# Kernel tuning notes

Hardware: AMD Instinct MI355X
Metric: run time of the kernel (lower is better)

The kernel has to match this reference:

```python
import jax, jax.numpy as jnp
import numpy as np

DIM = 768
HEADS = 12
HEAD_DIM = DIM // HEADS  # 64
THETA = 10000.0
B, S = 2, 2048


def rotate_half(x):
    # pairs-interleaved rotate: (x1, x2) -> (-x2, x1)
    xp = x.reshape(x.shape[:-1] + (-1, 2))
    x1, x2 = xp[..., 0], xp[..., 1]
    return jnp.stack((-x2, x1), axis=-1).reshape(x.shape)


def rope_freqs(seq_len, head_dim, dtype):
    inv = 1.0 / (THETA ** (jnp.arange(0, head_dim, 2, dtype=jnp.float32) / head_dim))
    pos = jnp.arange(seq_len, dtype=jnp.float32)
    f = pos[:, None] * inv[None, :]              # [S, head_dim//2]
    f = jnp.repeat(f, 2, axis=-1)                # [S, head_dim]
    return f.astype(dtype)


def apply_rotary(freqs, t):
    # freqs [S, D] broadcasts against t [B, H, S, D]
    return t * jnp.cos(freqs) + rotate_half(t) * jnp.sin(freqs)


def setup_inputs() -> dict:
    key = jax.random.key(0)
    k1, k2, k3 = jax.random.split(key, 3)
    x = jax.random.normal(k1, (B, S, DIM), dtype=jnp.float32)
    W_qkv = jax.random.normal(k2, (3 * DIM, DIM), dtype=jnp.float32) * 0.02
    W_proj = jax.random.normal(k3, (DIM, DIM), dtype=jnp.float32) * 0.02
    b_proj = jnp.zeros((DIM,), dtype=jnp.float32)
    return {"x": x, "W_qkv": W_qkv, "W_proj": W_proj, "b_proj": b_proj}


def reference(x, W_qkv, W_proj, b_proj):
    Bb, Ss, C = x.shape
    qkv = jnp.einsum('bsc,oc->bso', x, W_qkv)                    # [B,S,3C]
    qkv = qkv.reshape(Bb, Ss, 3, HEADS, HEAD_DIM)
    qkv = jnp.transpose(qkv, (2, 0, 3, 1, 4))                    # [3,B,H,S,D]
    q, k, v = qkv[0], qkv[1], qkv[2]
    freqs = rope_freqs(Ss, HEAD_DIM, x.dtype)
    q = apply_rotary(freqs, q)
    k = apply_rotary(freqs, k)
    scale = HEAD_DIM ** -0.5
    scores = jnp.einsum('bhqd,bhkd->bhqk', q, k) * scale         # [B,H,S,S]
    probs = jax.nn.softmax(scores, axis=-1)
    out = jnp.einsum('bhqk,bhkd->bhqd', probs, v)                # [B,H,S,D]
    out = jnp.transpose(out, (0, 2, 1, 3)).reshape(Bb, Ss, C)
    return jnp.einsum('bsc,oc->bso', out, W_proj) + b_proj
```

## Files before the change

kernel.cpp:

```cpp
#include <hip/hip_runtime.h>
#include <math.h>

#define Bq 2
#define Sq 2048
#define Cq 768
#define Hq 12
#define Dq 64

#define PANEL_SHORTS 98304
#define PANELS_X  32
#define PANELS_WQ 18
#define PANELS_WP 6

#define NROWS 49152
#define OPHALF 3145728

typedef _Float16 f16x8 __attribute__((ext_vector_type(8)));
typedef __fp16 fp16v2 __attribute__((ext_vector_type(2)));
typedef float f32x4 __attribute__((ext_vector_type(4)));
#define MFMA16F(a, b, c) __builtin_amdgcn_mfma_f32_16x16x32_f16(a, b, c, 0, 0, 0)

#define SCALEQ 0.18033688011112042f

static __device__ inline unsigned short f16bits(float x) {
    _Float16 h = (_Float16)x;
    return __builtin_bit_cast(unsigned short, h);
}
static __device__ inline unsigned int pk16(float a, float b) {
    fp16v2 h = __builtin_amdgcn_cvt_pkrtz(a, b);
    return __builtin_bit_cast(unsigned int, h);
}

static __device__ inline void gld_lds16(const unsigned short* g, unsigned short* l) {
    __builtin_amdgcn_global_load_lds(
        (const __attribute__((address_space(1))) unsigned int*)g,
        (__attribute__((address_space(3))) unsigned int*)l, 16, 0, 0);
}

__global__ void freq_kernel(float* __restrict__ ctab, float* __restrict__ stab) {
    int idx = blockIdx.x * blockDim.x + threadIdx.x;
    int s = idx >> 5;
    int i = idx & 31;
    double f = (double)s * exp(-(double)i * 0.28782313662425573);
    ctab[idx] = (float)cos(f);
    stab[idx] = (float)sin(f);
}

__global__ __launch_bounds__(256) void split_kernel(
    const float* __restrict__ x, const float* __restrict__ wq,
    const float* __restrict__ wp,
    unsigned short* __restrict__ xs, unsigned short* __restrict__ wqs,
    unsigned short* __restrict__ wps)
{
    const int cid  = blockIdx.x * 256 + threadIdx.x;
    const int panel = cid / 12288;
    const int pos8  = cid % 12288;
    const int step = pos8 >> 10;
    const int rem  = pos8 & 1023;
    const int J    = rem >> 6;
    const int lane = rem & 63;
    const int rowp = J * 8 + (lane >> 3);
    const int lc   = (lane & 7) ^ (rowp & 7);
    const int k    = step * 64 + lc * 8;
    const float* src; unsigned short* dst; int prow;
    if (panel < PANELS_X) {
        src = x;  dst = xs;  prow = panel;
    } else if (panel < PANELS_X + PANELS_WQ) {
        src = wq; dst = wqs; prow = panel - PANELS_X;
    } else {
        src = wp; dst = wps; prow = panel - PANELS_X - PANELS_WQ;
    }
    const int row = prow * 128 + rowp;
    float4 v0 = *(const float4*)(src + (size_t)row * Cq + k);
    float4 v1 = *(const float4*)(src + (size_t)row * Cq + k + 4);
    unsigned short o[8] = { f16bits(v0.x), f16bits(v0.y), f16bits(v0.z),
                            f16bits(v0.w), f16bits(v1.x), f16bits(v1.y),
                            f16bits(v1.z), f16bits(v1.w) };
    *(uint4*)&dst[(size_t)prow * PANEL_SHORTS + (size_t)pos8 * 8] = *(uint4*)o;
}

template <int MODE, int BM, int BN>
__global__ __launch_bounds__(256) void gemm_mfma_kernel(
    const unsigned short* __restrict__ Apr, const unsigned short* __restrict__ Bpr,
    const float* __restrict__ ctab, const float* __restrict__ stab,
    unsigned short* __restrict__ qp, unsigned short* __restrict__ kp,
    unsigned short* __restrict__ vp,
    float* __restrict__ out0, const float* __restrict__ bias)
{
    constexpr int MI  = BM / 32;
    constexpr int NI  = BN / 32;
    constexpr int WTM = BM / 2;
    constexpr int WTN = BN / 2;
    constexpr int BCH = BN / 8;
    constexpr int ACH = BM / 8;
    constexpr int CPW = (ACH + BCH) / 4;

    __shared__ unsigned short sA[BM * 64];
    __shared__ unsigned short sB[BN * 64];

    const int t    = threadIdx.x;
    const int w    = t >> 6;
    const int lane = t & 63;
    const int ml   = lane & 15;
    const int quad = lane >> 4;
    const int wm   = w >> 1;
    const int wn   = w & 1;

    const int mBase = blockIdx.y * BM;
    const int nBase = blockIdx.x * BN;

    const unsigned short* gpanA = Apr + (size_t)(mBase >> 7) * PANEL_SHORTS;
    const unsigned short* gpanB = Bpr + (size_t)(nBase >> 7) * PANEL_SHORTS;
    const int JbA = (mBase & 127) >> 3;
    const int JbB = (nBase & 127) >> 3;

    f32x4 acc[MI][NI];
    #pragma unroll
    for (int mi = 0; mi < MI; ++mi)
        #pragma unroll
        for (int ni = 0; ni < NI; ++ni)
            acc[mi][ni] = (f32x4){0.f, 0.f, 0.f, 0.f};

    for (int k0 = 0; k0 < 12; ++k0) {
        __syncthreads();
        #pragma unroll
        for (int cc = 0; cc < CPW; ++cc) {
            const int c = w * CPW + cc;
            if (c < BCH) {
                gld_lds16(gpanB + k0 * 8192 + (JbB + c) * 512 + lane * 8,
                          sB + c * 512);
            } else {
                const int a = c - BCH;
                gld_lds16(gpanA + k0 * 8192 + (JbA + a) * 512 + lane * 8,
                          sA + a * 512);
            }
        }
        __syncthreads();

        f16x8 aF[MI][2], bF[NI][2];
        #pragma unroll
        for (int mi = 0; mi < MI; ++mi) {
            const int row = wm * WTM + mi * 16 + ml;
            #pragma unroll
            for (int ks = 0; ks < 2; ++ks)
                aF[mi][ks] = *(const f16x8*)
                    &sA[row * 64 + (((ks * 4 + quad) ^ (row & 7)) << 3)];
        }
        #pragma unroll
        for (int ni = 0; ni < NI; ++ni) {
            const int row = wn * WTN + ni * 16 + ml;
            #pragma unroll
            for (int ks = 0; ks < 2; ++ks)
                bF[ni][ks] = *(const f16x8*)
                    &sB[row * 64 + (((ks * 4 + quad) ^ (row & 7)) << 3)];
        }
        #pragma unroll
        for (int mi = 0; mi < MI; ++mi)
            #pragma unroll
            for (int ni = 0; ni < NI; ++ni) {
                acc[mi][ni] = MFMA16F(aF[mi][0], bF[ni][0], acc[mi][ni]);
                acc[mi][ni] = MFMA16F(aF[mi][1], bF[ni][1], acc[mi][ni]);
            }
    }

    if (MODE == 0) {
        const int which = nBase / Cq;
        #pragma unroll
        for (int mi = 0; mi < MI; ++mi) {
            const int gm = mBase + wm * WTM + mi * 16 + quad * 4;
            const int bb = gm >> 11;
            const int s0 = gm & 2047;
            #pragma unroll
            for (int ni = 0; ni < NI; ++ni) {
                const int gn = nBase + wn * WTN + ni * 16 + ml;
                const int c  = gn - which * Cq;
                const int hh = c >> 6;
                const int dd = c & 63;
                const size_t hb = (size_t)(bb * Hq + hh);
                if (which < 2) {
                    #pragma unroll
                    for (int r = 0; r < 4; ++r) {
                        float val = acc[mi][ni][r];
                        float pv  = __shfl_xor(val, 1, 64);
                        const int fi = (s0 + r) * 32 + (dd >> 1);
                        float c0 = ctab[fi], sn = stab[fi];
                        float o = (dd & 1) ? (val * c0 + pv * sn)
                                           : (val * c0 - pv * sn);
                        if (which == 0) {
                            o *= SCALEQ;
                            qp[(hb * Sq + s0 + r) * 64 + dd] = f16bits(o);
                        } else {
                            const int ss = s0 + r, rr = ss & 63, kt2 = ss >> 6;
                            kp[(hb * 32 + kt2) * 4096 + rr * 64
                               + (((dd >> 3) ^ (rr & 7)) << 3) + (dd & 7)] = f16bits(o);
                        }
                    }
                } else {
                    unsigned short hv[4];
                    #pragma unroll
                    for (int r = 0; r < 4; ++r)
                        hv[r] = f16bits(acc[mi][ni][r]);
                    const int kt2 = s0 >> 6;
                    *(ushort4*)&vp[(hb * 32 + kt2) * 4096 + dd * 64
                        + ((((s0 & 63) >> 3) ^ (dd & 7)) << 3) + (s0 & 7)]
                        = *(ushort4*)hv;
                }
            }
        }
    } else {
        #pragma unroll
        for (int mi = 0; mi < MI; ++mi) {
            const int gm = mBase + wm * WTM + mi * 16 + quad * 4;
            #pragma unroll
            for (int ni = 0; ni < NI; ++ni) {
                const int gn = nBase + wn * WTN + ni * 16 + ml;
                const float bz = bias[gn];
                #pragma unroll
                for (int r = 0; r < 4; ++r)
                    out0[(size_t)(gm + r) * Cq + gn] = acc[mi][ni][r] + bz;
            }
        }
    }
}

__global__ __launch_bounds__(256, 6) void attn_mfma_kernel(
    const unsigned short* __restrict__ qp, const unsigned short* __restrict__ kp,
    const unsigned short* __restrict__ vp, unsigned short* __restrict__ op,
    float2* __restrict__ mlp)
{
    __shared__ __align__(16) unsigned short smem[12288];
    unsigned short* pb = smem + 8192;

    const int t    = threadIdx.x;
    const int w    = t >> 6;
    const int lane = t & 63;
    const int ml   = lane & 15;
    const int quad = lane >> 4;
    const int bi   = blockIdx.x;
    const int bh   = bi % 24;
    const int rest = bi / 24;
    const int qt   = rest >> 1;
    const int half = rest & 1;

    const bool isV = (w >= 2);
    const unsigned short* gsrc = isV ? vp : kp;
    const int Jb = (w & 1) * 4;
    const size_t gb = (size_t)bh * 131072;
    unsigned short* sdst = smem + (isV ? 4096 : 0);

    const size_t qrow = ((size_t)bh * Sq + qt * 64 + w * 16 + ml) * 64;
    f16x8 bQ[2];
    bQ[0] = *(const f16x8*)(qp + qrow + quad * 8);
    bQ[1] = *(const f16x8*)(qp + qrow + 32 + quad * 8);

    float m_st = -INFINITY, l_st = 0.f;
    f32x4 O[4];
    #pragma unroll
    for (int ng = 0; ng < 4; ++ng) O[ng] = (f32x4){0.f, 0.f, 0.f, 0.f};

    unsigned short* pbl = pb + (w * 16 + ml) * 64;
    const int rsw = ml & 7;

    const unsigned short* k_s = smem;
    const unsigned short* v_s = smem + 4096;

    for (int kt16 = 0; kt16 < 16; ++kt16) {
        const int kt = half * 16 + kt16;
        __syncthreads();
        {
            const unsigned short* gt = gsrc + gb + (size_t)kt * 4096;
            #pragma unroll
            for (int j = 0; j < 4; ++j)
                gld_lds16(gt + (Jb + j) * 512 + lane * 8, sdst + (Jb + j) * 512);
        }
        __syncthreads();

        f32x4 S[4];
        #pragma unroll
        for (int ng = 0; ng < 4; ++ng) {
            const int row = ng * 16 + ml;
            f32x4 acc = (f32x4){0.f, 0.f, 0.f, 0.f};
            #pragma unroll
            for (int ks = 0; ks < 2; ++ks) {
                f16x8 aK = *(const f16x8*)
                    &k_s[row * 64 + (((ks * 4 + quad) ^ (row & 7)) << 3)];
                acc = MFMA16F(aK, bQ[ks], acc);
            }
            S[ng] = acc;
        }

        float a0 = fmaxf(fmaxf(S[0][0], S[0][1]), fmaxf(S[0][2], S[0][3]));
        float a1 = fmaxf(fmaxf(S[1][0], S[1][1]), fmaxf(S[1][2], S[1][3]));
        float a2 = fmaxf(fmaxf(S[2][0], S[2][1]), fmaxf(S[2][2], S[2][3]));
        float a3 = fmaxf(fmaxf(S[3][0], S[3][1]), fmaxf(S[3][2], S[3][3]));
        float mx = fmaxf(fmaxf(a0, a1), fmaxf(a2, a3));
        mx = fmaxf(mx, __shfl_xor(mx, 16, 64));
        mx = fmaxf(mx, __shfl_xor(mx, 32, 64));
        if (__any(mx > m_st + 11.f)) {
            float nm = fmaxf(m_st, mx);
            float al = exp2f(m_st - nm);
            #pragma unroll
            for (int ng = 0; ng < 4; ++ng) O[ng] = O[ng] * al;
            l_st *= al;
            m_st = nm;
        }

        float ps = 0.f;
        #pragma unroll
        for (int ng = 0; ng < 4; ++ng) {
            float p0 = exp2f(S[ng][0] - m_st);
            float p1 = exp2f(S[ng][1] - m_st);
            float p2 = exp2f(S[ng][2] - m_st);
            float p3 = exp2f(S[ng][3] - m_st);
            ps += (p0 + p1) + (p2 + p3);
            uint2 u;
            u.x = pk16(p0, p1);
            u.y = pk16(p2, p3);
            const int ch = ng * 2 + (quad >> 1);
            *(uint2*)&pbl[((ch ^ rsw) << 3) + (quad & 1) * 4] = u;
        }
        ps += __shfl_xor(ps, 16, 64);
        ps += __shfl_xor(ps, 32, 64);
        l_st += ps;

        #pragma unroll
        for (int ks = 0; ks < 2; ++ks) {
            uint4 pu = *(const uint4*)&pbl[(((ks * 4 + quad) ^ rsw) << 3)];
            f16x8 bP = __builtin_bit_cast(f16x8, pu);
            #pragma unroll
            for (int ngd = 0; ngd < 4; ++ngd) {
                const int row = ngd * 16 + ml;
                f16x8 aV = *(const f16x8*)
                    &v_s[row * 64 + (((ks * 4 + quad) ^ (row & 7)) << 3)];
                O[ngd] = MFMA16F(aV, bP, O[ngd]);
            }
        }
    }

    const int srow = qt * 64 + w * 16 + ml;
    const size_t rowb = (size_t)half * NROWS + (size_t)bh * 2048 + srow;
    if (quad == 0) mlp[rowb] = make_float2(m_st, l_st);
    const float il = 1.0f / l_st;
    #pragma unroll
    for (int ngd = 0; ngd < 4; ++ngd) {
        unsigned short o4[4];
        #pragma unroll
        for (int r = 0; r < 4; ++r)
            o4[r] = f16bits(O[ngd][r] * il);
        *(ushort4*)&op[rowb * 64 + ngd * 16 + quad * 4] = *(ushort4*)o4;
    }
}

__global__ __launch_bounds__(256) void combine_kernel(
    const unsigned short* __restrict__ op, const float2* __restrict__ mlp,
    unsigned short* __restrict__ attns)
{
    const int g   = blockIdx.x * 256 + threadIdx.x;
    const int row = g >> 3;
    const int ch  = g & 7;
    const int bh  = row >> 11;
    const int s   = row & 2047;

    const float2 ml1 = mlp[row];
    const float2 ml2 = mlp[NROWS + row];
    const float M  = fmaxf(ml1.x, ml2.x);
    const float a1 = ml1.y * exp2f(ml1.x - M);
    const float a2 = ml2.y * exp2f(ml2.x - M);
    const float inv = 1.0f / (a1 + a2);
    const float c1 = a1 * inv, c2 = a2 * inv;

    f16x8 h1 = *(const f16x8*)(op + (size_t)row * 64 + ch * 8);
    f16x8 h2 = *(const f16x8*)(op + OPHALF + (size_t)row * 64 + ch * 8);
    unsigned short o[8];
    #pragma unroll
    for (int j = 0; j < 8; ++j)
        o[j] = f16bits(c1 * (float)h1[j] + c2 * (float)h2[j]);

    const int bb = bh / Hq, hh = bh % Hq;
    const int mrow = bb * 2048 + s;
    const int panel = mrow >> 7, r128 = mrow & 127;
    const size_t addr = (size_t)panel * PANEL_SHORTS
                      + (r128 >> 3) * 512 + (r128 & 7) * 64
                      + (size_t)hh * 8192
                      + ((ch ^ (r128 & 7)) << 3);
    *(uint4*)&attns[addr] = *(uint4*)o;
}

extern "C" void kernel_launch(void* const* d_in, const int* in_sizes, int n_in,
                              void* d_out, int out_size, void* d_ws, size_t ws_size,
                              hipStream_t stream) {
    const float* x     = (const float*)d_in[0];
    const float* Wqkv  = (const float*)d_in[1];
    const float* Wproj = (const float*)d_in[2];
    const float* bproj = (const float*)d_in[3];
    float* out = (float*)d_out;

    char* p = (char*)d_ws;
    unsigned short* xs    = (unsigned short*)p; p += (size_t)PANELS_X  * PANEL_SHORTS * 2;
    unsigned short* wqs   = (unsigned short*)p; p += (size_t)PANELS_WQ * PANEL_SHORTS * 2;
    unsigned short* wps   = (unsigned short*)p; p += (size_t)PANELS_WP * PANEL_SHORTS * 2;
    unsigned short* qp    = (unsigned short*)p; p += (size_t)24 * Sq * 64 * 2;
    unsigned short* kp    = (unsigned short*)p; p += (size_t)24 * 131072 * 2;
    unsigned short* vp    = (unsigned short*)p; p += (size_t)24 * 131072 * 2;
    unsigned short* attns = (unsigned short*)p; p += (size_t)PANELS_X * PANEL_SHORTS * 2;
    unsigned short* op    = (unsigned short*)p; p += (size_t)2 * OPHALF * 2;
    float2* mlp           = (float2*)p;         p += (size_t)2 * NROWS * 8;
    float* ctab = (float*)p; p += (size_t)Sq * 32 * 4;
    float* stab = (float*)p; p += (size_t)Sq * 32 * 4;

    freq_kernel<<<256, 256, 0, stream>>>(ctab, stab);
    split_kernel<<<(PANELS_X + PANELS_WQ + PANELS_WP) * 12288 / 256, 256, 0, stream>>>(
        x, Wqkv, Wproj, xs, wqs, wps);
    gemm_mfma_kernel<0, 64, 128><<<dim3(18, 64), 256, 0, stream>>>(
        xs, wqs, ctab, stab, qp, kp, vp, nullptr, nullptr);
    attn_mfma_kernel<<<dim3(24 * 64), 256, 0, stream>>>(qp, kp, vp, op, mlp);
    combine_kernel<<<dim3(1536), 256, 0, stream>>>(op, mlp, attns);
    gemm_mfma_kernel<1, 64, 64><<<dim3(12, 64), 256, 0, stream>>>(
        attns, wps, ctab, stab, nullptr, nullptr, nullptr, out, bproj);
}
```

Measured before the change: 183.5 us.

## Double per-wave query rows in attention and fold freq table into split kernel

The attention kernel drops to 128 threads per block, with each wave handling 32 query rows instead of 16. Each K and V fragment read from LDS now feeds two MFMAs, and each wave loads the full K or V tile. This is meant to cut LDS reads per MFMA and improve reuse, at the cost of higher register pressure and fewer waves to hide latency. Separately, the freq/cos/sin table kernel is merged into the split kernel as extra blocks to save one launch.

```diff
diff --git a/kernel.cpp b/kernel.cpp
--- a/kernel.cpp
+++ b/kernel.cpp
@@ -14,6 +14,7 @@
 
 #define NROWS 49152
 #define OPHALF 3145728
+#define SPLIT_BLOCKS 2688
 
 typedef _Float16 f16x8 __attribute__((ext_vector_type(8)));
 typedef __fp16 fp16v2 __attribute__((ext_vector_type(2)));
@@ -37,21 +38,22 @@
         (__attribute__((address_space(3))) unsigned int*)l, 16, 0, 0);
 }
 
-__global__ void freq_kernel(float* __restrict__ ctab, float* __restrict__ stab) {
-    int idx = blockIdx.x * blockDim.x + threadIdx.x;
-    int s = idx >> 5;
-    int i = idx & 31;
-    double f = (double)s * exp(-(double)i * 0.28782313662425573);
-    ctab[idx] = (float)cos(f);
-    stab[idx] = (float)sin(f);
-}
-
 __global__ __launch_bounds__(256) void split_kernel(
     const float* __restrict__ x, const float* __restrict__ wq,
     const float* __restrict__ wp,
     unsigned short* __restrict__ xs, unsigned short* __restrict__ wqs,
-    unsigned short* __restrict__ wps)
+    unsigned short* __restrict__ wps,
+    float* __restrict__ ctab, float* __restrict__ stab)
 {
+    if (blockIdx.x >= SPLIT_BLOCKS) {
+        int idx = (blockIdx.x - SPLIT_BLOCKS) * 256 + threadIdx.x;
+        int s = idx >> 5;
+        int i = idx & 31;
+        double f = (double)s * exp(-(double)i * 0.28782313662425573);
+        ctab[idx] = (float)cos(f);
+        stab[idx] = (float)sin(f);
+        return;
+    }
     const int cid  = blockIdx.x * 256 + threadIdx.x;
     const int panel = cid / 12288;
     const int pos8  = cid % 12288;
@@ -223,7 +225,7 @@
     }
 }
 
-__global__ __launch_bounds__(256, 6) void attn_mfma_kernel(
+__global__ __launch_bounds__(128, 3) void attn_mfma_kernel(
     const unsigned short* __restrict__ qp, const unsigned short* __restrict__ kp,
     const unsigned short* __restrict__ vp, unsigned short* __restrict__ op,
     float2* __restrict__ mlp)
@@ -242,23 +244,30 @@
     const int qt   = rest >> 1;
     const int half = rest & 1;
 
-    const bool isV = (w >= 2);
+    const bool isV = (w == 1);
     const unsigned short* gsrc = isV ? vp : kp;
-    const int Jb = (w & 1) * 4;
     const size_t gb = (size_t)bh * 131072;
     unsigned short* sdst = smem + (isV ? 4096 : 0);
 
-    const size_t qrow = ((size_t)bh * Sq + qt * 64 + w * 16 + ml) * 64;
-    f16x8 bQ[2];
-    bQ[0] = *(const f16x8*)(qp + qrow + quad * 8);
-    bQ[1] = *(const f16x8*)(qp + qrow + 32 + quad * 8);
-
-    float m_st = -INFINITY, l_st = 0.f;
-    f32x4 O[4];
+    f16x8 bQ[2][2];
     #pragma unroll
-    for (int ng = 0; ng < 4; ++ng) O[ng] = (f32x4){0.f, 0.f, 0.f, 0.f};
-
-    unsigned short* pbl = pb + (w * 16 + ml) * 64;
+    for (int qf = 0; qf < 2; ++qf) {
+        const size_t qrow =
+            ((size_t)bh * Sq + qt * 64 + w * 32 + qf * 16 + ml) * 64;
+        bQ[qf][0] = *(const f16x8*)(qp + qrow + quad * 8);
+        bQ[qf][1] = *(const f16x8*)(qp + qrow + 32 + quad * 8);
+    }
+
+    float m0 = -INFINITY, m1 = -INFINITY, l0 = 0.f, l1 = 0.f;
+    f32x4 O0[4], O1[4];
+    #pragma unroll
+    for (int ng = 0; ng < 4; ++ng) {
+        O0[ng] = (f32x4){0.f, 0.f, 0.f, 0.f};
+        O1[ng] = (f32x4){0.f, 0.f, 0.f, 0.f};
+    }
+
+    unsigned short* pbl0 = pb + (w * 32 + ml) * 64;
+    unsigned short* pbl1 = pbl0 + 16 * 64;
     const int rsw = ml & 7;
 
     const unsigned short* k_s = smem;
@@ -270,84 +279,115 @@
         {
             const unsigned short* gt = gsrc + gb + (size_t)kt * 4096;
             #pragma unroll
-            for (int j = 0; j < 4; ++j)
-                gld_lds16(gt + (Jb + j) * 512 + lane * 8, sdst + (Jb + j) * 512);
+            for (int j = 0; j < 8; ++j)
+                gld_lds16(gt + j * 512 + lane * 8, sdst + j * 512);
         }
         __syncthreads();
 
-        f32x4 S[4];
+        f32x4 S0[4], S1[4];
         #pragma unroll
         for (int ng = 0; ng < 4; ++ng) {
             const int row = ng * 16 + ml;
-            f32x4 acc = (f32x4){0.f, 0.f, 0.f, 0.f};
+            f32x4 a0 = (f32x4){0.f, 0.f, 0.f, 0.f};
+            f32x4 a1 = (f32x4){0.f, 0.f, 0.f, 0.f};
             #pragma unroll
             for (int ks = 0; ks < 2; ++ks) {
                 f16x8 aK = *(const f16x8*)
                     &k_s[row * 64 + (((ks * 4 + quad) ^ (row & 7)) << 3)];
-                acc = MFMA16F(aK, bQ[ks], acc);
-            }
-            S[ng] = acc;
-        }
-
-        float a0 = fmaxf(fmaxf(S[0][0], S[0][1]), fmaxf(S[0][2], S[0][3]));
-        float a1 = fmaxf(fmaxf(S[1][0], S[1][1]), fmaxf(S[1][2], S[1][3]));
-        float a2 = fmaxf(fmaxf(S[2][0], S[2][1]), fmaxf(S[2][2], S[2][3]));
-        float a3 = fmaxf(fmaxf(S[3][0], S[3][1]), fmaxf(S[3][2], S[3][3]));
-        float mx = fmaxf(fmaxf(a0, a1), fmaxf(a2, a3));
-        mx = fmaxf(mx, __shfl_xor(mx, 16, 64));
-        mx = fmaxf(mx, __shfl_xor(mx, 32, 64));
-        if (__any(mx > m_st + 11.f)) {
-            float nm = fmaxf(m_st, mx);
-            float al = exp2f(m_st - nm);
-            #pragma unroll
-            for (int ng = 0; ng < 4; ++ng) O[ng] = O[ng] * al;
-            l_st *= al;
-            m_st = nm;
-        }
-
-        float ps = 0.f;
+                a0 = MFMA16F(aK, bQ[0][ks], a0);
+                a1 = MFMA16F(aK, bQ[1][ks], a1);
+            }
+            S0[ng] = a0; S1[ng] = a1;
+        }
+
+        float x0 = fmaxf(fmaxf(fmaxf(S0[0][0], S0[0][1]), fmaxf(S0[0][2], S0[0][3])),
+                         fmaxf(fmaxf(S0[1][0], S0[1][1]), fmaxf(S0[1][2], S0[1][3])));
+        float y0 = fmaxf(fmaxf(fmaxf(S0[2][0], S0[2][1]), fmaxf(S0[2][2], S0[2][3])),
+                         fmaxf(fmaxf(S0[3][0], S0[3][1]), fmaxf(S0[3][2], S0[3][3])));
+        float x1 = fmaxf(fmaxf(fmaxf(S1[0][0], S1[0][1]), fmaxf(S1[0][2], S1[0][3])),
+                         fmaxf(fmaxf(S1[1][0], S1[1][1]), fmaxf(S1[1][2], S1[1][3])));
+        float y1 = fmaxf(fmaxf(fmaxf(S1[2][0], S1[2][1]), fmaxf(S1[2][2], S1[2][3])),
+                         fmaxf(fmaxf(S1[3][0], S1[3][1]), fmaxf(S1[3][2], S1[3][3])));
+        float mx0 = fmaxf(x0, y0);
+        float mx1 = fmaxf(x1, y1);
+        mx0 = fmaxf(mx0, __shfl_xor(mx0, 16, 64));
+        mx1 = fmaxf(mx1, __shfl_xor(mx1, 16, 64));
+        mx0 = fmaxf(mx0, __shfl_xor(mx0, 32, 64));
+        mx1 = fmaxf(mx1, __shfl_xor(mx1, 32, 64));
+        if (__any((mx0 > m0 + 11.f) || (mx1 > m1 + 11.f))) {
+            float nm0 = fmaxf(m0, mx0), nm1 = fmaxf(m1, mx1);
+            float al0 = exp2f(m0 - nm0), al1 = exp2f(m1 - nm1);
+            #pragma unroll
+            for (int ng = 0; ng < 4; ++ng) {
+                O0[ng] = O0[ng] * al0;
+                O1[ng] = O1[ng] * al1;
+            }
+            l0 *= al0; l1 *= al1;
+            m0 = nm0;  m1 = nm1;
+        }
+
+        float ps0 = 0.f, ps1 = 0.f;
         #pragma unroll
         for (int ng = 0; ng < 4; ++ng) {
-            float p0 = exp2f(S[ng][0] - m_st);
-            float p1 = exp2f(S[ng][1] - m_st);
-            float p2 = exp2f(S[ng][2] - m_st);
-            float p3 = exp2f(S[ng][3] - m_st);
-            ps += (p0 + p1) + (p2 + p3);
-            uint2 u;
-            u.x = pk16(p0, p1);
-            u.y = pk16(p2, p3);
             const int ch = ng * 2 + (quad >> 1);
-            *(uint2*)&pbl[((ch ^ rsw) << 3) + (quad & 1) * 4] = u;
-        }
-        ps += __shfl_xor(ps, 16, 64);
-        ps += __shfl_xor(ps, 32, 64);
-        l_st += ps;
+            const int off = ((ch ^ rsw) << 3) + (quad & 1) * 4;
+            float p00 = exp2f(S0[ng][0] - m0);
+            float p01 = exp2f(S0[ng][1] - m0);
+            float p02 = exp2f(S0[ng][2] - m0);
+            float p03 = exp2f(S0[ng][3] - m0);
+            ps0 += (p00 + p01) + (p02 + p03);
+            uint2 u0; u0.x = pk16(p00, p01); u0.y = pk16(p02, p03);
+            *(uint2*)&pbl0[off] = u0;
+            float p10 = exp2f(S1[ng][0] - m1);
+            float p11 = exp2f(S1[ng][1] - m1);
+            float p12 = exp2f(S1[ng][2] - m1);
+            float p13 = exp2f(S1[ng][3] - m1);
+            ps1 += (p10 + p11) + (p12 + p13);
+            uint2 u1; u1.x = pk16(p10, p11); u1.y = pk16(p12, p13);
+            *(uint2*)&pbl1[off] = u1;
+        }
+        ps0 += __shfl_xor(ps0, 16, 64);
+        ps1 += __shfl_xor(ps1, 16, 64);
+        ps0 += __shfl_xor(ps0, 32, 64);
+        ps1 += __shfl_xor(ps1, 32, 64);
+        l0 += ps0; l1 += ps1;
 
         #pragma unroll
         for (int ks = 0; ks < 2; ++ks) {
-            uint4 pu = *(const uint4*)&pbl[(((ks * 4 + quad) ^ rsw) << 3)];
-            f16x8 bP = __builtin_bit_cast(f16x8, pu);
+            const int poff = ((ks * 4 + quad) ^ rsw) << 3;
+            uint4 pu0 = *(const uint4*)&pbl0[poff];
+            uint4 pu1 = *(const uint4*)&pbl1[poff];
+            f16x8 bP0 = __builtin_bit_cast(f16x8, pu0);
+            f16x8 bP1 = __builtin_bit_cast(f16x8, pu1);
             #pragma unroll
             for (int ngd = 0; ngd < 4; ++ngd) {
                 const int row = ngd * 16 + ml;
                 f16x8 aV = *(const f16x8*)
                     &v_s[row * 64 + (((ks * 4 + quad) ^ (row & 7)) << 3)];
-                O[ngd] = MFMA16F(aV, bP, O[ngd]);
-            }
-        }
-    }
-
-    const int srow = qt * 64 + w * 16 + ml;
-    const size_t rowb = (size_t)half * NROWS + (size_t)bh * 2048 + srow;
-    if (quad == 0) mlp[rowb] = make_float2(m_st, l_st);
-    const float il = 1.0f / l_st;
+                O0[ngd] = MFMA16F(aV, bP0, O0[ngd]);
+                O1[ngd] = MFMA16F(aV, bP1, O1[ngd]);
+            }
+        }
+    }
+
     #pragma unroll
-    for (int ngd = 0; ngd < 4; ++ngd) {
-        unsigned short o4[4];
-        #pragma unroll
-        for (int r = 0; r < 4; ++r)
-            o4[r] = f16bits(O[ngd][r] * il);
-        *(ushort4*)&op[rowb * 64 + ngd * 16 + quad * 4] = *(ushort4*)o4;
+    for (int qf = 0; qf < 2; ++qf) {
+        const int srow = qt * 64 + w * 32 + qf * 16 + ml;
+        const size_t rowb = (size_t)half * NROWS + (size_t)bh * 2048 + srow;
+        const float mq = qf ? m1 : m0;
+        const float lq = qf ? l1 : l0;
+        if (quad == 0) mlp[rowb] = make_float2(mq, lq);
+        const float il = 1.0f / lq;
+        #pragma unroll
+        for (int ngd = 0; ngd < 4; ++ngd) {
+            unsigned short o4[4];
+            #pragma unroll
+            for (int r = 0; r < 4; ++r) {
+                float ov = qf ? O1[ngd][r] : O0[ngd][r];
+                o4[r] = f16bits(ov * il);
+            }
+            *(ushort4*)&op[rowb * 64 + ngd * 16 + quad * 4] = *(ushort4*)o4;
+        }
     }
 }
 
@@ -408,12 +448,11 @@
     float* ctab = (float*)p; p += (size_t)Sq * 32 * 4;
     float* stab = (float*)p; p += (size_t)Sq * 32 * 4;
 
-    freq_kernel<<<256, 256, 0, stream>>>(ctab, stab);
-    split_kernel<<<(PANELS_X + PANELS_WQ + PANELS_WP) * 12288 / 256, 256, 0, stream>>>(
-        x, Wqkv, Wproj, xs, wqs, wps);
+    split_kernel<<<SPLIT_BLOCKS + 256, 256, 0, stream>>>(
+        x, Wqkv, Wproj, xs, wqs, wps, ctab, stab);
     gemm_mfma_kernel<0, 64, 128><<<dim3(18, 64), 256, 0, stream>>>(
         xs, wqs, ctab, stab, qp, kp, vp, nullptr, nullptr);
-    attn_mfma_kernel<<<dim3(24 * 64), 256, 0, stream>>>(qp, kp, vp, op, mlp);
+    attn_mfma_kernel<<<dim3(24 * 64), 128, 0, stream>>>(qp, kp, vp, op, mlp);
     combine_kernel<<<dim3(1536), 256, 0, stream>>>(op, mlp, attns);
     gemm_mfma_kernel<1, 64, 64><<<dim3(12, 64), 256, 0, stream>>>(
         attns, wps, ctab, stab, nullptr, nullptr, nullptr, out, bproj);
```

New measurement: 181.6 us. About the same (-1.1%).
